# Performance work log

Hardware: AMD Instinct MI355X
Metric: run time of the kernel (lower is better)

Reference implementation:

```python
import jax, jax.numpy as jnp
import numpy as np

HEADS = 8

def setup_inputs() -> dict:
    key = jax.random.key(0)
    ks = jax.random.split(key, 5)
    B, S, C = 2, 4096, 640
    s = 1.0 / np.sqrt(C)
    return {
        "hidden_states": jax.random.normal(ks[0], (B, S, C), dtype=jnp.float32),
        "Wq": jax.random.normal(ks[1], (C, C), dtype=jnp.float32) * s,
        "bq": jnp.zeros((C,), dtype=jnp.float32),
        "Wk": jax.random.normal(ks[2], (C, C), dtype=jnp.float32) * s,
        "bk": jnp.zeros((C,), dtype=jnp.float32),
        "Wv": jax.random.normal(ks[3], (C, C), dtype=jnp.float32) * s,
        "bv": jnp.zeros((C,), dtype=jnp.float32),
        "Wo": jax.random.normal(ks[4], (C, C), dtype=jnp.float32) * s,
        "bo": jnp.zeros((C,), dtype=jnp.float32),
    }


def reference(hidden_states, Wq, bq, Wk, bk, Wv, bv, Wo, bo):
    # Self-attention (encoder_hidden_states=None), no mask, no norms.
    B, S, C = hidden_states.shape
    H = HEADS
    D = C // H  # head_dim
    residual = hidden_states

    q = hidden_states @ Wq + bq  # [B,S,C]
    k = hidden_states @ Wk + bk
    v = hidden_states @ Wv + bv

    # [B,S,C] -> [B,H,S,D]
    q = q.reshape(B, S, H, D).transpose(0, 2, 1, 3)
    k = k.reshape(B, S, H, D).transpose(0, 2, 1, 3)
    v = v.reshape(B, S, H, D).transpose(0, 2, 1, 3)

    scale = 1.0 / np.sqrt(D)
    scores = jnp.einsum('bhqd,bhkd->bhqk', q, k) * scale  # [B,H,S,S]
    probs = jax.nn.softmax(scores, axis=-1)               # materialized, as in source
    out = jnp.einsum('bhqk,bhkd->bhqd', probs, v)         # [B,H,S,D]

    out = out.transpose(0, 2, 1, 3).reshape(B, S, C)
    out = out @ Wo + bo  # to_out[0]; to_out[1] is dropout (identity in eval)
    out = out + residual  # residual_connection=True
    return out            # rescale_output_factor = 1.0
```

## Files before the change

### kernel.cpp

```cpp
#include <hip/hip_runtime.h>
#include <hip/hip_bf16.h>
#include <stdint.h>

typedef __attribute__((ext_vector_type(8))) short short8;
typedef __attribute__((ext_vector_type(4))) short short4v;
typedef __attribute__((ext_vector_type(4))) float f32x4;
typedef __attribute__((ext_vector_type(16))) float f32x16;
typedef unsigned short u16;
typedef unsigned int u32;

#define DEV __device__ __forceinline__

constexpr int Bb = 2, Ss = 4096, Cc = 640, Hh = 8, Dd = 80;
constexpr int BS = Bb * Ss;
constexpr int NQKV = 3 * Cc;
constexpr int QKst = 2 * Cc;

DEV float bf2f(u16 u) { unsigned v = ((unsigned)u) << 16; float f; __builtin_memcpy(&f, &v, 4); return f; }
DEV u16 f2bf(float f) {
    unsigned u; __builtin_memcpy(&u, &f, 4);
    u += 0x7fffu + ((u >> 16) & 1u);
    return (u16)(u >> 16);
}
DEV u32 packbf2(float a, float b) {
    float2 f2; f2.x = a; f2.y = b;
    __hip_bfloat162 h2 = __float22bfloat162_rn(f2);
    u32 r; __builtin_memcpy(&r, &h2, 4);
    return r;
}

DEV void pswapf(float &a, float &b) {
#if __has_builtin(__builtin_amdgcn_permlane32_swap)
    auto r = __builtin_amdgcn_permlane32_swap(__float_as_int(a), __float_as_int(b), false, false);
    a = __int_as_float(r[0]); b = __int_as_float(r[1]);
#else
    float sa = __shfl_xor(a, 32, 64), sb = __shfl_xor(b, 32, 64);
    bool hi = (threadIdx.x & 32) != 0;
    float na = hi ? sb : a, nb = hi ? b : sa;
    a = na; b = nb;
#endif
}

#define GLD16(gp, lp) __builtin_amdgcn_global_load_lds( \
    (const __attribute__((address_space(1))) void*)(gp), \
    (__attribute__((address_space(3))) void*)(lp), 16, 0, 0)

__global__ __launch_bounds__(256) void prep_kernel(
    const float* __restrict__ hs,
    const float* __restrict__ Wq, const float* __restrict__ Wk,
    const float* __restrict__ Wv, const float* __restrict__ Wo,
    const float* __restrict__ bq, const float* __restrict__ bk,
    const float* __restrict__ bv,
    u16* __restrict__ Xb, float* __restrict__ bcat,
    u16* __restrict__ WTqkv, u16* __restrict__ WTo)
{
    const float QS = 0.11180339887498949f * 1.4426950408889634f;
    if (blockIdx.x < 1600) {
        __shared__ float T[32][33];
        int tile = blockIdx.x;
        int wsel = tile / 400;
        int tt = tile - wsel * 400;
        int tr = tt / 20, tc = tt - (tt / 20) * 20;
        const float* W = (wsel == 0) ? Wq : (wsel == 1) ? Wk : (wsel == 2) ? Wv : Wo;
        float sc = (wsel == 0) ? QS : 1.0f;
        int r = threadIdx.x >> 3, c4 = (threadIdx.x & 7) * 4;
        float4 v = *(const float4*)(W + (size_t)(tr * 32 + r) * Cc + tc * 32 + c4);
        T[r][c4 + 0] = v.x; T[r][c4 + 1] = v.y; T[r][c4 + 2] = v.z; T[r][c4 + 3] = v.w;
        __syncthreads();
        short4v o;
#pragma unroll
        for (int j = 0; j < 4; j++) o[j] = (short)f2bf(T[c4 + j][r] * sc);
        u16* dst = (wsel < 3) ? (WTqkv + (size_t)(wsel * Cc + tc * 32 + r) * Cc + tr * 32 + c4)
                              : (WTo + (size_t)(tc * 32 + r) * Cc + tr * 32 + c4);
        *(short4v*)dst = o;
    } else {
        int tid = (blockIdx.x - 1600) * blockDim.x + threadIdx.x;
        int nthr = 2048 * blockDim.x;
        for (int i = tid; i < BS * Cc / 4; i += nthr) {
            float4 v = ((const float4*)hs)[i];
            short4v o;
            o[0] = (short)f2bf(v.x); o[1] = (short)f2bf(v.y);
            o[2] = (short)f2bf(v.z); o[3] = (short)f2bf(v.w);
            ((short4v*)Xb)[i] = o;
        }
        for (int i = tid; i < NQKV; i += nthr) {
            float v = (i < Cc) ? bq[i] * QS : (i < 2 * Cc) ? bk[i - Cc] : bv[i - 2 * Cc];
            bcat[i] = v;
        }
    }
}

__global__ __launch_bounds__(256) void gemm_qkv(
    const u16* __restrict__ A, const u16* __restrict__ Bt,
    const float* __restrict__ bias, u16* __restrict__ QK,
    u16* __restrict__ VTg)
{
    __shared__ __align__(16) char gsm[32768];

    const int mBase = blockIdx.x * 128;
    const int nBase = blockIdx.y * 128;
    const int t = threadIdx.x, lane = t & 63, w = t >> 6;
    const int wr = w >> 1, wc = w & 1;
    const int l15 = lane & 15, g = lane >> 4;

    const int r0 = t >> 2, r1 = (t + 256) >> 2;
    const int cg0 = (t & 3) ^ (r0 & 3);
    const int cg1 = (t & 3) ^ (r1 & 3);
    const u16* pa0 = A + (size_t)(mBase + r0) * Cc + cg0 * 8;
    const u16* pa1 = A + (size_t)(mBase + r1) * Cc + cg1 * 8;
    const u16* pb0 = Bt + (size_t)(nBase + r0) * Cc + cg0 * 8;
    const u16* pb1 = Bt + (size_t)(nBase + r1) * Cc + cg1 * 8;

    auto stage = [&](int k0, int buf) {
        GLD16(pa0 + k0, gsm + buf * 8192 + w * 1024);
        GLD16(pa1 + k0, gsm + buf * 8192 + 4096 + w * 1024);
        GLD16(pb0 + k0, gsm + 16384 + buf * 8192 + w * 1024);
        GLD16(pb1 + k0, gsm + 16384 + buf * 8192 + 4096 + w * 1024);
    };

    stage(0, 0);
    __syncthreads();

    f32x4 acc[4][4] = {};
    const int lof = l15 * 64 + ((g ^ (l15 & 3)) << 4);
    int cur = 0;

    for (int k0 = 0; k0 < Cc; k0 += 32) {
        if (k0 + 32 < Cc) stage(k0 + 32, cur ^ 1);
        short8 af[4], bf[4];
#pragma unroll
        for (int i = 0; i < 4; i++) {
            af[i] = *(const short8*)(gsm + cur * 8192 + wr * 4096 + i * 1024 + lof);
            bf[i] = *(const short8*)(gsm + 16384 + cur * 8192 + wc * 4096 + i * 1024 + lof);
        }
#pragma unroll
        for (int mi = 0; mi < 4; mi++)
#pragma unroll
            for (int ni = 0; ni < 4; ni++)
                acc[mi][ni] = __builtin_amdgcn_mfma_f32_16x16x32_bf16(af[mi], bf[ni], acc[mi][ni], 0, 0, 0);
        __syncthreads();
        cur ^= 1;
    }

    if (nBase < 2 * Cc) {
#pragma unroll
        for (int mi = 0; mi < 4; mi++)
#pragma unroll
            for (int ni = 0; ni < 4; ni++) {
                int col = nBase + wc * 64 + ni * 16 + l15;
                float bb = bias[col];
#pragma unroll
                for (int r = 0; r < 4; r++) {
                    int row = mBase + wr * 64 + mi * 16 + g * 4 + r;
                    QK[(size_t)row * QKst + col] = f2bf(acc[mi][ni][r] + bb);
                }
            }
    } else {
        const int gp = ((g & 1) << 1) | (g >> 1);
#pragma unroll
        for (int mi = 0; mi < 4; mi++)
#pragma unroll
            for (int ni = 0; ni < 4; ni++) {
                int colg = nBase + wc * 64 + ni * 16 + l15;
                float bb = bias[colg];
                int vc = colg - 2 * Cc;
                int h = vc / Dd, d = vc - h * Dd;
                int row0 = mBase + wr * 64 + mi * 16 + gp * 4;
                int b = (mBase >> 12), s = row0 & 4095;
                short4v o;
#pragma unroll
                for (int r = 0; r < 4; r++) o[r] = (short)f2bf(acc[mi][ni][r] + bb);
                *(short4v*)(VTg + ((size_t)(b * Hh + h) * Dd + d) * Ss + s) = o;
            }
    }
}

constexpr int OBP = 88;

__global__ __launch_bounds__(256, 3) void attn_kernel(
    const u16* __restrict__ QK, const u16* __restrict__ VTg,
    u16* __restrict__ N0, u16* __restrict__ N1,
    float* __restrict__ Mp, float* __restrict__ Lp)
{
    __shared__ __align__(16) char smem[45056];

    const int id = blockIdx.x;
    const int qt = id >> 5;
    const int bh = (id & 31) >> 1;
    const int kvs = id & 1;
    const int b = bh >> 3, h = bh & 7;
    const int t = threadIdx.x, lane = t & 63, w = t >> 6;
    const int l31 = lane & 31, e = lane >> 5;

    const size_t rowBase = (size_t)b * Ss;
    const int q0 = qt * 128;
    const int kvBase = kvs * (Ss / 2);
    constexpr int NT = (Ss / 2) / 64;

    const int lq8 = lane >> 3;
    const int vcg = (lane & 7) ^ lq8;
    const u16* kg0 = QK + (rowBase + kvBase + lane) * QKst + Cc + h * Dd;
    const u16* vg0 = VTg + ((size_t)bh * Dd) * Ss + kvBase + vcg * 8;

    for (int i = t; i < 512; i += 256) {
        ((u32*)(smem + 10240 + 80 * 128))[i] = 0x3F803F80u;
        ((u32*)(smem + 22528 + 10240 + 80 * 128))[i] = 0x3F803F80u;
    }

    short8 qB[5];
    {
        const u16* qp = QK + (rowBase + q0 + w * 32 + l31) * QKst + h * Dd + e * 8;
#pragma unroll
        for (int ks = 0; ks < 5; ks++) qB[ks] = *(const short8*)(qp + ks * 16);
    }

    auto stageK = [&](int kt, int buf) {
#pragma unroll
        for (int j = 0; j < 3; j++) {
            int gi = w + 4 * j;
            if (gi < 10)
                GLD16(kg0 + (size_t)kt * 64 * QKst + gi * 8,
                      smem + buf * 22528 + gi * 1024);
        }
    };
    auto stageV = [&](int kt, int buf) {
#pragma unroll
        for (int j = 0; j < 3; j++) {
            int gi = w + 4 * j;
            if (gi < 10)
                GLD16(vg0 + (size_t)(gi * 8 + lq8) * Ss + kt * 64,
                      smem + buf * 22528 + 10240 + gi * 1024);
        }
    };

    stageK(0, 0);
    stageV(0, 0);
    stageK(1, 1);
    stageV(1, 1);
    __syncthreads();

    float mrow = -1e30f;
    f32x16 oacc[3] = {};
    const int csl_base = l31 & 7;

    for (int kt = 0; kt < NT; ++kt) {
        const char* kb = smem + (kt & 1) * 22528;
        const char* vb = kb + 10240;

        f32x16 s2[2];
        __builtin_amdgcn_s_setprio(1);
#pragma unroll
        for (int n = 0; n < 2; n++) {
            f32x16 a = {};
#pragma unroll
            for (int ks = 0; ks < 5; ks++) {
                short8 kf = *(const short8*)(kb + ((2 * ks + e) * 64 + n * 32 + l31) * 16);
                a = __builtin_amdgcn_mfma_f32_32x32x16_bf16(kf, qB[ks], a, 0, 0, 0);
            }
            s2[n] = a;
        }
        __builtin_amdgcn_s_setprio(0);

#define SV(j) ((j) < 16 ? s2[0][(j)] : s2[1][(j) - 16])
        float tt[11];
#pragma unroll
        for (int i = 0; i < 10; i++)
            tt[i] = fmaxf(fmaxf(SV(3 * i), SV(3 * i + 1)), SV(3 * i + 2));
        tt[10] = fmaxf(SV(30), SV(31));
#undef SV
        float u0 = fmaxf(fmaxf(tt[0], tt[1]), tt[2]);
        float u1 = fmaxf(fmaxf(tt[3], tt[4]), tt[5]);
        float u2 = fmaxf(fmaxf(tt[6], tt[7]), tt[8]);
        float u3 = fmaxf(tt[9], tt[10]);
        float vm = fmaxf(fmaxf(u0, u1), fmaxf(u2, u3));
        { float va = vm, vb2 = vm; pswapf(va, vb2); vm = fmaxf(va, vb2); }

        if (__any(vm > mrow + 8.0f)) {
            float mnew = fmaxf(mrow, vm);
            float al = __builtin_amdgcn_exp2f(mrow - mnew);
            mrow = mnew;
#pragma unroll
            for (int n = 0; n < 3; n++)
#pragma unroll
                for (int r = 0; r < 16; r++) oacc[n][r] *= al;
        }

        u32 pd[2][8];
#pragma unroll
        for (int n = 0; n < 2; n++)
#pragma unroll
            for (int m = 0; m < 8; m++) {
                float pa = __builtin_amdgcn_exp2f(s2[n][2 * m] - mrow);
                float pb = __builtin_amdgcn_exp2f(s2[n][2 * m + 1] - mrow);
                pd[n][m] = packbf2(pa, pb);
            }

        __builtin_amdgcn_s_setprio(1);
#pragma unroll
        for (int ks = 0; ks < 4; ks++) {
            const int n = ks >> 1, bb2 = ks & 1;
            union { u32 u[4]; short8 v; } pB;
            pB.u[0] = pd[n][4 * bb2 + 0];
            pB.u[1] = pd[n][4 * bb2 + 1];
            pB.u[2] = pd[n][4 * bb2 + 2];
            pB.u[3] = pd[n][4 * bb2 + 3];
            const int csl = (2 * ks + e) ^ csl_base;
#pragma unroll
            for (int n2 = 0; n2 < 3; n2++) {
                short8 vf = *(const short8*)(vb + ((n2 * 32 + l31) * 8 + csl) * 16);
                oacc[n2] = __builtin_amdgcn_mfma_f32_32x32x16_bf16(vf, pB.v, oacc[n2], 0, 0, 0);
            }
        }
        __builtin_amdgcn_s_setprio(0);

        __syncthreads();
        if (kt + 2 < NT) {
            stageK(kt + 2, kt & 1);
            stageV(kt + 2, kt & 1);
        }
    }

    if (e == 0) {
        int mi = kvs * 65536 + bh * Ss + q0 + w * 32 + l31;
        Mp[mi] = mrow;
        Lp[mi] = oacc[2][8];
    }

    u16* Ob = (u16*)smem;
#pragma unroll
    for (int n = 0; n < 3; n++)
#pragma unroll
        for (int r = 0; r < 16; r += 2) {
            if (n == 2 && r >= 8) continue;
            int dloc = n * 32 + (r & 3) + 8 * (r >> 2) + 4 * e;
            u32 pk = packbf2(oacc[n][r], oacc[n][r + 1]);
            *(u32*)&Ob[(w * 32 + l31) * OBP + dloc] = pk;
        }
    __syncthreads();

    u16* Np = kvs ? N1 : N0;
    const int cb = h * Dd;
#pragma unroll
    for (int i = 0; i < 5; i++) {
        int gidx = i * 256 + t;
        int row = gidx / 10, gi = gidx % 10;
        short8 v = *(const short8*)&Ob[row * OBP + gi * 8];
        *(short8*)(Np + (rowBase + q0 + row) * Cc + cb + gi * 8) = v;
    }
}

__global__ __launch_bounds__(256) void gemm_oproj(
    const u16* __restrict__ N0, const u16* __restrict__ N1,
    const u16* __restrict__ Bt,
    const float* __restrict__ Mp, const float* __restrict__ Lp,
    const float* __restrict__ bias, const float* __restrict__ resid,
    float* __restrict__ Out)
{
    __shared__ __align__(16) char osm[28672];
    float* WF = (float*)(osm + 24576);

    const int mBase = blockIdx.x * 64;
    const int nBase = blockIdx.y * 128;
    const int t = threadIdx.x, lane = t & 63, w = t >> 6;
    const int wr = w >> 1, wc = w & 1;
    const int l15 = lane & 15, g = lane >> 4;

    for (int i = t; i < 512; i += 256) {
        int r = i >> 3, h = i & 7;
        int row = mBase + r;
        int bb = row >> 12, q = row & 4095;
        int mi = (bb * 8 + h) * Ss + q;
        float m0 = Mp[mi], m1 = Mp[65536 + mi];
        float l0 = Lp[mi], l1 = Lp[65536 + mi];
        float m = fmaxf(m0, m1);
        float w0 = exp2f(m0 - m), w1 = exp2f(m1 - m);
        float rl = 1.0f / (l0 * w0 + l1 * w1);
        WF[(r * 8 + h) * 2 + 0] = w0 * rl;
        WF[(r * 8 + h) * 2 + 1] = w1 * rl;
    }

    const int rA = t >> 2, clA = t & 3;
    const int cgA = clA ^ (rA & 3);
    const int rB0 = t >> 2, rB1 = (t + 256) >> 2;
    const int cgB0 = (t & 3) ^ (rB0 & 3);
    const int cgB1 = (t & 3) ^ (rB1 & 3);
    const u16* pA0 = N0 + (size_t)(mBase + rA) * Cc + cgA * 8;
    const u16* pA1 = N1 + (size_t)(mBase + rA) * Cc + cgA * 8;
    const u16* pB0 = Bt + (size_t)(nBase + rB0) * Cc + cgB0 * 8;
    const u16* pB1 = Bt + (size_t)(nBase + rB1) * Cc + cgB1 * 8;

    auto stageB = [&](int k0, int buf) {
        GLD16(pB0 + k0, osm + 8192 + buf * 8192 + w * 1024);
        GLD16(pB1 + k0, osm + 8192 + buf * 8192 + 4096 + w * 1024);
    };
    auto stageA = [&](int k0, int buf) {
        int kA = k0 + cgA * 8;
        int hA = kA / 80;
        float w0 = WF[(rA * 8 + hA) * 2], w1 = WF[(rA * 8 + hA) * 2 + 1];
        short8 a0 = *(const short8*)(pA0 + k0);
        short8 c0 = *(const short8*)(pA1 + k0);
        union { u32 u[4]; short8 v; } mg;
#pragma unroll
        for (int j = 0; j < 4; j++)
            mg.u[j] = packbf2(bf2f((u16)a0[2 * j]) * w0 + bf2f((u16)c0[2 * j]) * w1,
                              bf2f((u16)a0[2 * j + 1]) * w0 + bf2f((u16)c0[2 * j + 1]) * w1);
        *(short8*)(osm + buf * 4096 + rA * 64 + clA * 16) = mg.v;
    };

    __syncthreads();
    stageB(0, 0);
    stageA(0, 0);
    __syncthreads();

    f32x4 acc[2][4] = {};
    const int lof = l15 * 64 + ((g ^ (l15 & 3)) << 4);
    int cur = 0;

    for (int k0 = 0; k0 < Cc; k0 += 32) {
        const bool more = (k0 + 32 < Cc);
        if (more) stageB(k0 + 32, cur ^ 1);
        short8 af[2], bf[4];
#pragma unroll
        for (int i = 0; i < 2; i++)
            af[i] = *(const short8*)(osm + cur * 4096 + wr * 2048 + i * 1024 + lof);
#pragma unroll
        for (int i = 0; i < 4; i++)
            bf[i] = *(const short8*)(osm + 8192 + cur * 8192 + wc * 4096 + i * 1024 + lof);
#pragma unroll
        for (int mi = 0; mi < 2; mi++)
#pragma unroll
            for (int ni = 0; ni < 4; ni++)
                acc[mi][ni] = __builtin_amdgcn_mfma_f32_16x16x32_bf16(af[mi], bf[ni], acc[mi][ni], 0, 0, 0);
        if (more) stageA(k0 + 32, cur ^ 1);
        __syncthreads();
        cur ^= 1;
    }

#pragma unroll
    for (int mi = 0; mi < 2; mi++)
#pragma unroll
        for (int ni = 0; ni < 4; ni++) {
            int col = nBase + wc * 64 + ni * 16 + l15;
            float bb = bias[col];
#pragma unroll
            for (int r = 0; r < 4; r++) {
                int row = mBase + wr * 32 + mi * 16 + g * 4 + r;
                Out[(size_t)row * Cc + col] = acc[mi][ni][r] + bb + resid[(size_t)row * Cc + col];
            }
        }
}

extern "C" void kernel_launch(void* const* d_in, const int* in_sizes, int n_in,
                              void* d_out, int out_size, void* d_ws, size_t ws_size,
                              hipStream_t stream) {
    (void)in_sizes; (void)n_in; (void)out_size; (void)ws_size;
    const float* hs = (const float*)d_in[0];
    const float* Wq = (const float*)d_in[1];
    const float* bq = (const float*)d_in[2];
    const float* Wk = (const float*)d_in[3];
    const float* bk = (const float*)d_in[4];
    const float* Wv = (const float*)d_in[5];
    const float* bv = (const float*)d_in[6];
    const float* Wo = (const float*)d_in[7];
    const float* bo = (const float*)d_in[8];
    float* out = (float*)d_out;

    char* ws = (char*)d_ws;
    u16*   Xb    = (u16*)  (ws + 0);
    u16*   WTqkv = (u16*)  (ws + 10485760);
    u16*   WTo   = (u16*)  (ws + 12943360);
    float* bcat  = (float*)(ws + 13762560);
    u16*   QK    = (u16*)  (ws + 13770240);
    u16*   VTg   = (u16*)  (ws + 34741760);
    u16*   AOb   = (u16*)  (ws + 45227520);
    float* Mp    = (float*)(ws + 55713280);
    float* Lp    = (float*)(ws + 56237568);
    u16*   N1    = Xb;

    prep_kernel<<<dim3(3648), dim3(256), 0, stream>>>(hs, Wq, Wk, Wv, Wo, bq, bk, bv,
                                                      Xb, bcat, WTqkv, WTo);
    gemm_qkv<<<dim3(64, 15), dim3(256), 0, stream>>>(Xb, WTqkv, bcat, QK, VTg);
    attn_kernel<<<dim3(1024), dim3(256), 0, stream>>>(QK, VTg, AOb, N1, Mp, Lp);
    gemm_oproj<<<dim3(128, 5), dim3(256), 0, stream>>>(AOb, N1, WTo, Mp, Lp, bo, hs, out);
}
```

Before: 177.8 us.

## Software-pipeline QK^T one tile ahead with triple-buffered K in attention

The attention loop now computes the score MFMAs for the next KV tile before running softmax and the PV product on the current tile. K moves to a three-slot shared-memory ring and V to its own two-slot ring, so K can be staged three tiles ahead. This is meant to hide softmax and exp latency behind matrix work. In exchange it needs more shared memory and 32 extra accumulator registers per lane, and launch bounds drop from 3 to 2 blocks per CU, which lowers occupancy.

```diff
diff --git a/kernel.cpp b/kernel.cpp
--- a/kernel.cpp
+++ b/kernel.cpp
@@ -177,12 +177,12 @@
 
 constexpr int OBP = 88;
 
-__global__ __launch_bounds__(256, 3) void attn_kernel(
+__global__ __launch_bounds__(256, 2) void attn_kernel(
     const u16* __restrict__ QK, const u16* __restrict__ VTg,
     u16* __restrict__ N0, u16* __restrict__ N1,
     float* __restrict__ Mp, float* __restrict__ Lp)
 {
-    __shared__ __align__(16) char smem[45056];
+    __shared__ __align__(16) char smem[55296];
 
     const int id = blockIdx.x;
     const int qt = id >> 5;
@@ -203,8 +203,8 @@
     const u16* vg0 = VTg + ((size_t)bh * Dd) * Ss + kvBase + vcg * 8;
 
     for (int i = t; i < 512; i += 256) {
-        ((u32*)(smem + 10240 + 80 * 128))[i] = 0x3F803F80u;
-        ((u32*)(smem + 22528 + 10240 + 80 * 128))[i] = 0x3F803F80u;
+        ((u32*)(smem + 30720 + 10240))[i] = 0x3F803F80u;
+        ((u32*)(smem + 30720 + 12288 + 10240))[i] = 0x3F803F80u;
     }
 
     short8 qB[5];
@@ -220,16 +220,16 @@
             int gi = w + 4 * j;
             if (gi < 10)
                 GLD16(kg0 + (size_t)kt * 64 * QKst + gi * 8,
-                      smem + buf * 22528 + gi * 1024);
+                      smem + buf * 10240 + gi * 1024);
         }
     };
-    auto stageV = [&](int kt, int buf) {
+    auto stageV = [&](int kt, int vb) {
 #pragma unroll
         for (int j = 0; j < 3; j++) {
             int gi = w + 4 * j;
             if (gi < 10)
                 GLD16(vg0 + (size_t)(gi * 8 + lq8) * Ss + kt * 64,
-                      smem + buf * 22528 + 10240 + gi * 1024);
+                      smem + 30720 + vb * 12288 + gi * 1024);
         }
     };
 
@@ -237,27 +237,44 @@
     stageV(0, 0);
     stageK(1, 1);
     stageV(1, 1);
+    stageK(2, 2);
     __syncthreads();
 
     float mrow = -1e30f;
     f32x16 oacc[3] = {};
     const int csl_base = l31 & 7;
 
-    for (int kt = 0; kt < NT; ++kt) {
-        const char* kb = smem + (kt & 1) * 22528;
-        const char* vb = kb + 10240;
-
-        f32x16 s2[2];
+    f32x16 s2[2];
+    {
         __builtin_amdgcn_s_setprio(1);
 #pragma unroll
         for (int n = 0; n < 2; n++) {
             f32x16 a = {};
 #pragma unroll
             for (int ks = 0; ks < 5; ks++) {
-                short8 kf = *(const short8*)(kb + ((2 * ks + e) * 64 + n * 32 + l31) * 16);
+                short8 kf = *(const short8*)(smem + ((2 * ks + e) * 64 + n * 32 + l31) * 16);
                 a = __builtin_amdgcn_mfma_f32_32x32x16_bf16(kf, qB[ks], a, 0, 0, 0);
             }
             s2[n] = a;
+        }
+        __builtin_amdgcn_s_setprio(0);
+    }
+
+    int kq = 1;
+    int kst = 0;
+    for (int kt = 0; kt < NT; ++kt) {
+        const char* kbn = smem + kq * 10240;
+        f32x16 s2n[2];
+        __builtin_amdgcn_s_setprio(1);
+#pragma unroll
+        for (int n = 0; n < 2; n++) {
+            f32x16 a = {};
+#pragma unroll
+            for (int ks = 0; ks < 5; ks++) {
+                short8 kf = *(const short8*)(kbn + ((2 * ks + e) * 64 + n * 32 + l31) * 16);
+                a = __builtin_amdgcn_mfma_f32_32x32x16_bf16(kf, qB[ks], a, 0, 0, 0);
+            }
+            s2n[n] = a;
         }
         __builtin_amdgcn_s_setprio(0);
 
@@ -295,6 +312,7 @@
                 pd[n][m] = packbf2(pa, pb);
             }
 
+        const char* vbp = smem + 30720 + (kt & 1) * 12288;
         __builtin_amdgcn_s_setprio(1);
 #pragma unroll
         for (int ks = 0; ks < 4; ks++) {
@@ -307,17 +325,19 @@
             const int csl = (2 * ks + e) ^ csl_base;
 #pragma unroll
             for (int n2 = 0; n2 < 3; n2++) {
-                short8 vf = *(const short8*)(vb + ((n2 * 32 + l31) * 8 + csl) * 16);
+                short8 vf = *(const short8*)(vbp + ((n2 * 32 + l31) * 8 + csl) * 16);
                 oacc[n2] = __builtin_amdgcn_mfma_f32_32x32x16_bf16(vf, pB.v, oacc[n2], 0, 0, 0);
             }
         }
         __builtin_amdgcn_s_setprio(0);
 
         __syncthreads();
-        if (kt + 2 < NT) {
-            stageK(kt + 2, kt & 1);
-            stageV(kt + 2, kt & 1);
-        }
+        if (kt + 3 < NT) stageK(kt + 3, kst);
+        if (kt + 2 < NT) stageV(kt + 2, kt & 1);
+        s2[0] = s2n[0];
+        s2[1] = s2n[1];
+        kq = (kq == 2) ? 0 : kq + 1;
+        kst = (kst == 2) ? 0 : kst + 1;
     }
 
     if (e == 0) {
```

After: 189.6 us. +6.6%, slower.
